# Optimization experiments

Hardware: AMD Instinct MI355X
Metric: run time of the kernel (lower is better)

Reference implementation:

```python
import jax, jax.numpy as jnp
import numpy as np

N = 50000   # nodes
E = 500000  # edges
D = 128     # enc_dim == Hout
INIT_W = 0.1


def _lin_w(k, din, dout):
    return jax.random.normal(k, (dout, din), jnp.float32) * INIT_W


def setup_inputs() -> dict:
    key = jax.random.key(0)
    ks = jax.random.split(key, 16)
    inp = {
        "x": jax.random.normal(ks[0], (N, D), jnp.float32),
        "src": jax.random.randint(ks[1], (E,), 0, N),
        "dst": jax.random.randint(ks[2], (E,), 0, N),
        # encoders (Linear enc_dim -> enc_dim)
        "WencK": _lin_w(ks[3], D, D), "bencK": jnp.zeros((D,), jnp.float32),
        "WencP1": _lin_w(ks[4], D, D), "bencP1": jnp.zeros((D,), jnp.float32),
        "WencP2": _lin_w(ks[5], D, D), "bencP2": jnp.zeros((D,), jnp.float32),
        # Kfun: Linear-Tanh-Linear-ReLU-Linear
        "K0W": _lin_w(ks[6], D, D), "K0b": jnp.zeros((D,), jnp.float32),
        "K1W": _lin_w(ks[7], D, D), "K1b": jnp.zeros((D,), jnp.float32),
        "K2W": _lin_w(ks[8], D, D), "K2b": jnp.zeros((D,), jnp.float32),
        # Ufun: Linear-Tanh-Linear-ReLU-Linear
        "U0W": _lin_w(ks[9], D, D), "U0b": jnp.zeros((D,), jnp.float32),
        "U1W": _lin_w(ks[10], D, D), "U1b": jnp.zeros((D,), jnp.float32),
        "U2W": _lin_w(ks[11], D, D), "U2b": jnp.zeros((D,), jnp.float32),
    }
    return inp


def _mlp3(h, W0, b0, W1, b1, W2, b2):
    h = jnp.tanh(h @ W0.T + b0)
    h = jax.nn.relu(h @ W1.T + b1)
    return h @ W2.T + b2


def reference(x, src, dst,
              WencK, bencK, WencP1, bencP1, WencP2, bencP2,
              K0W, K0b, K1W, K1b, K2W, K2b,
              U0W, U0b, U1W, U1b, U2W, U2b):
    # getK: encode nodes, copy_u + sum to dst, node MLP
    h1 = x @ WencK.T + bencK                                   # [N, D]
    h1_agg = jax.ops.segment_sum(h1[src], dst, num_segments=N)  # [N, D]
    Knode = _mlp3(h1_agg, K0W, K0b, K1W, K1b, K2W, K2b)         # [N, D]
    # getU: u_add_v on encoded features, edge MLP
    p1 = x @ WencP1.T + bencP1
    p2 = x @ WencP2.T + bencP2
    Eedge = _mlp3(p1[src] + p2[dst], U0W, U0b, U1W, U1b, U2W, U2b)  # [E, D]
    # getH: u_mul_e + sum to dst
    Enew = jax.ops.segment_sum(Knode[src] * Eedge, dst, num_segments=N)  # [N, D]
    return jnp.sum(Enew)
```

## Files before the change

kernel.cpp:

```cpp
#include <hip/hip_runtime.h>
#include <hip/hip_bf16.h>
#include <math.h>

#define NN 50000
#define NE 500000
#define DD 128
#define STR 136
#define NSCAN (2 * NN)
#define SCAN_BLK ((NSCAN + 1023) / 1024)
#define HIST_BLK ((NE + 255) / 256)
#define CVT_BLK  ((NN * DD + 4095) / 4096)
#define PRECONV_BLK ((7 * 2048 + 1023) / 1024)
#define ENC_BLK  ((NN + 127) / 128)

typedef __attribute__((ext_vector_type(8))) short short8;
typedef __attribute__((ext_vector_type(4))) float floatx4;

__device__ __forceinline__ float bf2f(unsigned short u) {
    unsigned v = ((unsigned)u) << 16;
    float f;
    __builtin_memcpy(&f, &v, 4);
    return f;
}
__device__ __forceinline__ unsigned short f2bf(float f) {
    unsigned x;
    __builtin_memcpy(&x, &f, 4);
    x += 0x7FFF + ((x >> 16) & 1);
    return (unsigned short)(x >> 16);
}
__device__ __forceinline__ float fast_tanh(float x) {
    float t = __builtin_amdgcn_exp2f(x * 2.88539008177793f);
    return 1.f - 2.f * __builtin_amdgcn_rcpf(t + 1.f);
}

__global__ __launch_bounds__(256) void k1_kernel(
    const int* __restrict__ src, const int* __restrict__ dst,
    int* __restrict__ cnt_dst, int* __restrict__ cnt_src,
    int* __restrict__ rank_d, int* __restrict__ rank_s,
    const float* __restrict__ x, unsigned short* __restrict__ xbf,
    const float* __restrict__ U0W, const float* __restrict__ WencP1,
    const float* __restrict__ WencP2, const float* __restrict__ K0W,
    const float* __restrict__ WencK,
    const float* __restrict__ bp1, const float* __restrict__ bp2,
    const float* __restrict__ U0b, const float* __restrict__ bk,
    const float* __restrict__ U2b,
    float* __restrict__ comp, float* __restrict__ bvecs)
{
    __shared__ float Bs[DD * DD];
    int blk = blockIdx.x;
    int t = threadIdx.x;

    if (blk < HIST_BLK) {
        int e = blk * 256 + t;
        if (e < NE) {
            rank_d[e] = atomicAdd(&cnt_dst[dst[e]], 1);
            rank_s[e] = atomicAdd(&cnt_src[src[e]], 1);
        }
        return;
    }
    if (blk < HIST_BLK + CVT_BLK) {
        int base = (blk - HIST_BLK) * 4096;
        #pragma unroll
        for (int j = 0; j < 4; ++j) {
            int idx = base + (j * 256 + t) * 4;
            if (idx < NN * DD) {
                float4 f = *(const float4*)&x[idx];
                ushort4 v4;
                v4.x = f2bf(f.x); v4.y = f2bf(f.y);
                v4.z = f2bf(f.z); v4.w = f2bf(f.w);
                *(ushort4*)&xbf[idx] = v4;
            }
        }
        return;
    }

    int b = blk - (HIST_BLK + CVT_BLK);
    if (b == 6) {
        if (t < 128) {
            float s1 = 0.f, s2 = 0.f;
            for (int k = 0; k < DD; ++k) {
                s1 += U0W[t * DD + k] * (bp1[k] + bp2[k]);
                s2 += K0W[t * DD + k] * bk[k];
            }
            bvecs[t] = s1 + U0b[t];
            bvecs[128 + t] = s2;
            int f = (t & 64) + 16 * (t & 3) + ((t & 63) >> 2);
            bvecs[256 + t] = U2b[f];
        }
        return;
    }
    int mat = b >> 1, half = b & 1;
    const float* A = (mat == 2) ? K0W : U0W;
    const float* B = (mat == 0) ? WencP1 : (mat == 1) ? WencP2 : WencK;
    float* C = comp + (size_t)mat * DD * DD;
    for (int i = 0; i < 64; ++i)
        Bs[i * 256 + t] = B[i * 256 + t];
    __syncthreads();
    int row = half * 64 + (t >> 2);
    int j0 = (t & 3) * 32;
    float acc[32];
    #pragma unroll
    for (int jj = 0; jj < 32; ++jj) acc[jj] = 0.f;
    for (int k = 0; k < DD; ++k) {
        float a = A[row * DD + k];
        #pragma unroll
        for (int jj = 0; jj < 32; ++jj)
            acc[jj] += a * Bs[k * DD + j0 + jj];
    }
    #pragma unroll
    for (int jj = 0; jj < 32; ++jj) C[row * DD + j0 + jj] = acc[jj];
}

__global__ __launch_bounds__(1024) void k2_kernel(
    const float* __restrict__ comp, const float* __restrict__ K1W,
    const float* __restrict__ K2W, const float* __restrict__ U2W,
    const float* __restrict__ U1W, unsigned short* __restrict__ wfrag,
    const int* __restrict__ cnt, int* __restrict__ base, int* __restrict__ bsum)
{
    int t = threadIdx.x;
    if (blockIdx.x < PRECONV_BLK) {
        int g = blockIdx.x * 1024 + t;
        if (g >= 7 * 2048) return;
        int m = g >> 11;
        int rem = g & 2047;
        int kt = rem >> 9, nt = (rem >> 6) & 7, lane = rem & 63;
        const float* W;
        bool perm = false, tr = false;
        switch (m) {
            case 0: W = comp; break;
            case 1: W = comp + 16384; break;
            case 2: W = comp + 32768; break;
            case 3: W = K1W; perm = true; break;
            case 4: W = K2W; perm = true; break;
            case 5: W = U2W; perm = true; tr = true; break;
            default: W = U1W; break;
        }
        int n = nt * 16 + (lane & 15);
        #pragma unroll
        for (int j = 0; j < 8; ++j) {
            int ks = kt * 32 + (lane >> 4) * 8 + j;
            int f = perm ? (ks & 64) + 16 * (ks & 3) + ((ks & 63) >> 2) : ks;
            float v = tr ? W[f * DD + n] : W[n * DD + f];
            wfrag[(size_t)g * 8 + j] = f2bf(v);
        }
        return;
    }
    __shared__ int wsum[16];
    int sb = blockIdx.x - PRECONV_BLK;
    int i = sb * 1024 + t;
    int v = (i < NSCAN) ? cnt[i] : 0;
    int lane = t & 63, w = t >> 6;
    int xv = v;
    #pragma unroll
    for (int off = 1; off < 64; off <<= 1) {
        int y = __shfl_up(xv, off);
        if (lane >= off) xv += y;
    }
    if (lane == 63) wsum[w] = xv;
    __syncthreads();
    if (w == 0) {
        int s = (lane < 16) ? wsum[lane] : 0;
        #pragma unroll
        for (int off = 1; off < 16; off <<= 1) {
            int y = __shfl_up(s, off);
            if (lane >= off) s += y;
        }
        if (lane < 16) wsum[lane] = s;
    }
    __syncthreads();
    int wavebase = (w == 0) ? 0 : wsum[w - 1];
    int incl = wavebase + xv;
    if (i < NSCAN) base[i] = incl - v;
    if (t == 1023) bsum[sb] = incl;
}

__global__ __launch_bounds__(128) void scan2_kernel(
    int* __restrict__ bsum, float* __restrict__ out)
{
    if (threadIdx.x == 0 && blockIdx.x == 0) *out = 0.f;
    __shared__ int wsum[2];
    int t = threadIdx.x;
    int v = (t < SCAN_BLK) ? bsum[t] : 0;
    int lane = t & 63, w = t >> 6;
    int x = v;
    #pragma unroll
    for (int off = 1; off < 64; off <<= 1) {
        int y = __shfl_up(x, off);
        if (lane >= off) x += y;
    }
    if (lane == 63) wsum[w] = x;
    __syncthreads();
    int wavebase = (w == 0) ? 0 : wsum[0];
    int incl = wavebase + x;
    if (t < SCAN_BLK) bsum[t] = incl - v;
}

__global__ __launch_bounds__(1024) void scan3_kernel(
    int* __restrict__ base, const int* __restrict__ bsum)
{
    int i = blockIdx.x * 1024 + threadIdx.x;
    if (i < NSCAN) base[i] += bsum[blockIdx.x];
}

__global__ __launch_bounds__(256) void place_kernel(
    const int* __restrict__ src, const int* __restrict__ dst,
    const int* __restrict__ base,
    const int* __restrict__ rank_d, const int* __restrict__ rank_s,
    int* __restrict__ sorted_src_bydst, int2* __restrict__ epairs)
{
    int e = blockIdx.x * 256 + threadIdx.x;
    if (e < NE) {
        int s = src[e], d = dst[e];
        sorted_src_bydst[base[d] + rank_d[e]] = s;
        int p = base[NN + s] + rank_s[e] - NE;
        epairs[p] = make_int2(s, d);
    }
}

__global__ __launch_bounds__(256) void agg_kernel(
    const unsigned short* __restrict__ xbf,
    const int* __restrict__ base, const int* __restrict__ cnt,
    const int* __restrict__ sorted_src,
    unsigned short* __restrict__ xagg)
{
    int wave = blockIdx.x * 4 + (threadIdx.x >> 6);
    int lane = threadIdx.x & 63;
    if (wave >= NN) return;
    int lo = base[wave];
    int hi = lo + cnt[wave];
    float ax = 0.f, ay = 0.f;
    for (int off = lo; off < hi; off += 64) {
        int myid = (off + lane < hi) ? sorted_src[off + lane] : 0;
        int nk = min(64, hi - off);
        int k = 0;
        for (; k + 4 <= nk; k += 4) {
            int s0 = __shfl(myid, k);
            int s1 = __shfl(myid, k + 1);
            int s2 = __shfl(myid, k + 2);
            int s3 = __shfl(myid, k + 3);
            ushort2 v0 = *(const ushort2*)&xbf[(size_t)s0 * DD + lane * 2];
            ushort2 v1 = *(const ushort2*)&xbf[(size_t)s1 * DD + lane * 2];
            ushort2 v2 = *(const ushort2*)&xbf[(size_t)s2 * DD + lane * 2];
            ushort2 v3 = *(const ushort2*)&xbf[(size_t)s3 * DD + lane * 2];
            ax += bf2f(v0.x) + bf2f(v1.x) + bf2f(v2.x) + bf2f(v3.x);
            ay += bf2f(v0.y) + bf2f(v1.y) + bf2f(v2.y) + bf2f(v3.y);
        }
        for (; k < nk; ++k) {
            int s = __shfl(myid, k);
            ushort2 v = *(const ushort2*)&xbf[(size_t)s * DD + lane * 2];
            ax += bf2f(v.x);
            ay += bf2f(v.y);
        }
    }
    ushort2 o;
    o.x = f2bf(ax); o.y = f2bf(ay);
    *(ushort2*)&xagg[(size_t)wave * DD + lane * 2] = o;
}

__global__ __launch_bounds__(256) void encnode_kernel(
    const float* __restrict__ x, const unsigned short* __restrict__ xagg,
    const unsigned short* __restrict__ wf, const float* __restrict__ bvecs,
    const int* __restrict__ cnt,
    const float* __restrict__ K0b, const float* __restrict__ K1b,
    const float* __restrict__ K2b,
    unsigned short* __restrict__ q1, unsigned short* __restrict__ q2,
    unsigned short* __restrict__ Km, float* __restrict__ kb)
{
    __shared__ unsigned short A[128 * STR];
    const int t = threadIdx.x;
    const int lane = t & 63, w = t >> 6;
    const int wm = w >> 1, wn = w & 1;
    const int c = lane & 15, q = lane >> 4;

    if (blockIdx.x < ENC_BLK) {
        const int row0 = blockIdx.x * 128;
        #pragma unroll
        for (int i = 0; i < 16; ++i) {
            int idx = i * 256 + t;
            int r = idx >> 5, ch = idx & 31;
            int gr = row0 + r;
            ushort4 v4 = {0, 0, 0, 0};
            if (gr < NN) {
                float4 f = *(const float4*)&x[(size_t)gr * DD + ch * 4];
                v4.x = f2bf(f.x); v4.y = f2bf(f.y);
                v4.z = f2bf(f.z); v4.w = f2bf(f.w);
            }
            *(ushort4*)&A[r * STR + ch * 4] = v4;
        }
        __syncthreads();

        for (int l = 0; l < 2; ++l) {
            floatx4 acc[4][4];
            #pragma unroll
            for (int i = 0; i < 4; ++i)
                #pragma unroll
                for (int j = 0; j < 4; ++j)
                    acc[i][j] = (floatx4){0.f, 0.f, 0.f, 0.f};
            const short8* W8 = (const short8*)(wf + (size_t)l * 16384);
            #pragma unroll
            for (int kt = 0; kt < 4; ++kt) {
                short8 af[4], bfr[4];
                #pragma unroll
                for (int i = 0; i < 4; ++i)
                    af[i] = *(const short8*)&A[(wm * 64 + i * 16 + c) * STR + kt * 32 + q * 8];
                #pragma unroll
                for (int j = 0; j < 4; ++j)
                    bfr[j] = W8[(kt * 8 + wn * 4 + j) * 64 + lane];
                #pragma unroll
                for (int i = 0; i < 4; ++i)
                    #pragma unroll
                    for (int j = 0; j < 4; ++j)
                        acc[i][j] = __builtin_amdgcn_mfma_f32_16x16x32_bf16(af[i], bfr[j], acc[i][j], 0, 0, 0);
            }
            unsigned short* pp = (l == 0) ? q1 : q2;
            float bv[4];
            #pragma unroll
            for (int j = 0; j < 4; ++j)
                bv[j] = (l == 0) ? bvecs[c + 16 * j + 64 * wn] : 0.f;

            #pragma unroll
            for (int i = 0; i < 4; ++i)
                #pragma unroll
                for (int r = 0; r < 4; ++r) {
                    int node = row0 + wm * 64 + i * 16 + 4 * q + r;
                    if (node < NN) {
                        #pragma unroll
                        for (int j = 0; j < 4; ++j)
                            pp[(size_t)node * DD + c + 16 * j + 64 * wn] = f2bf(acc[i][j][r] + bv[j]);
                    }
                }
        }
        return;
    }

    const int row0 = (blockIdx.x - ENC_BLK) * 128;
    #pragma unroll
    for (int i = 0; i < 8; ++i) {
        int idx = i * 256 + t;
        int r = idx >> 4, ch = idx & 15;
        int gr = row0 + r;
        short8 v = (short8){0,0,0,0,0,0,0,0};
        if (gr < NN) v = *(const short8*)&xagg[(size_t)gr * DD + ch * 8];
        *(short8*)&A[r * STR + ch * 8] = v;
    }
    __syncthreads();

    for (int l = 0; l < 4; ++l) {
        floatx4 acc[4][4];
        #pragma unroll
        for (int i = 0; i < 4; ++i)
            #pragma unroll
            for (int j = 0; j < 4; ++j)
                acc[i][j] = (floatx4){0.f, 0.f, 0.f, 0.f};
        const short8* W8 = (const short8*)(wf + (size_t)(2 + l) * 16384);
        #pragma unroll
        for (int kt = 0; kt < 4; ++kt) {
            short8 af[4], bfr[4];
            #pragma unroll
            for (int i = 0; i < 4; ++i)
                af[i] = *(const short8*)&A[(wm * 64 + i * 16 + c) * STR + kt * 32 + q * 8];
            #pragma unroll
            for (int j = 0; j < 4; ++j)
                bfr[j] = W8[(kt * 8 + wn * 4 + j) * 64 + lane];
            #pragma unroll
            for (int i = 0; i < 4; ++i)
                #pragma unroll
                for (int j = 0; j < 4; ++j)
                    acc[i][j] = __builtin_amdgcn_mfma_f32_16x16x32_bf16(af[i], bfr[j], acc[i][j], 0, 0, 0);
        }

        if (l < 3) {
            const float* bb = (l == 0) ? K0b : (l == 1) ? K1b : K2b;
            float bv[4];
            #pragma unroll
            for (int j = 0; j < 4; ++j) bv[j] = bb[c + 16 * j + 64 * wn];
            float bvv[4];
            #pragma unroll
            for (int j = 0; j < 4; ++j)
                bvv[j] = (l == 0) ? bvecs[128 + c + 16 * j + 64 * wn] : 0.f;

            __syncthreads();
            #pragma unroll
            for (int i = 0; i < 4; ++i)
                #pragma unroll
                for (int r = 0; r < 4; ++r) {
                    int node = row0 + wm * 64 + i * 16 + 4 * q + r;
                    float cn = (l == 0) ? (float)((node < NN) ? cnt[node] : 0) : 0.f;
                    float v0 = acc[i][0][r] + bv[0] + cn * bvv[0];
                    float v1 = acc[i][1][r] + bv[1] + cn * bvv[1];
                    float v2 = acc[i][2][r] + bv[2] + cn * bvv[2];
                    float v3 = acc[i][3][r] + bv[3] + cn * bvv[3];
                    if (l == 0) {
                        v0 = fast_tanh(v0); v1 = fast_tanh(v1);
                        v2 = fast_tanh(v2); v3 = fast_tanh(v3);
                    } else if (l == 1) {
                        v0 = fmaxf(v0, 0.f); v1 = fmaxf(v1, 0.f);
                        v2 = fmaxf(v2, 0.f); v3 = fmaxf(v3, 0.f);
                    }
                    ushort4 pk;
                    pk.x = f2bf(v0); pk.y = f2bf(v1); pk.z = f2bf(v2); pk.w = f2bf(v3);
                    int m = wm * 64 + i * 16 + 4 * q + r;
                    *(ushort4*)&A[m * STR + 4 * c + 64 * wn] = pk;
                }
            __syncthreads();

            if (l == 2) {
                if (t < 128) {
                    int node = row0 + t;
                    if (node < NN) {
                        float s = 0.f;
                        #pragma unroll
                        for (int ch = 0; ch < 16; ++ch) {
                            short8 v = *(const short8*)&A[t * STR + ch * 8];
                            #pragma unroll
                            for (int e = 0; e < 8; ++e)
                                s += bf2f((unsigned short)v[e]) * bvecs[256 + ch * 8 + e];
                        }
                        kb[node] = s;
                    }
                }
            }
        } else {
            #pragma unroll
            for (int i = 0; i < 4; ++i)
                #pragma unroll
                for (int r = 0; r < 4; ++r) {
                    int node = row0 + wm * 64 + i * 16 + 4 * q + r;
                    if (node < NN) {
                        ushort4 pk;
                        pk.x = f2bf(acc[i][0][r]);
                        pk.y = f2bf(acc[i][1][r]);
                        pk.z = f2bf(acc[i][2][r]);
                        pk.w = f2bf(acc[i][3][r]);
                        *(ushort4*)&Km[(size_t)node * DD + 4 * c + 64 * wn] = pk;
                    }
                }
        }
    }
}

__global__ __launch_bounds__(256) void edge_kernel(
    const unsigned short* __restrict__ q1, const unsigned short* __restrict__ q2,
    const unsigned short* __restrict__ Km, const float* __restrict__ kb,
    const int2* __restrict__ epairs,
    const unsigned short* __restrict__ wf, const float* __restrict__ U1b,
    float* __restrict__ out)
{
    __shared__ unsigned short A[128 * STR];
    __shared__ int sidx[128];
    __shared__ int didx[128];
    __shared__ float red[4];
    const int t = threadIdx.x;
    const int lane = t & 63, w = t >> 6;
    const int wm = w >> 1, wn = w & 1;
    const int c = lane & 15, q = lane >> 4;

    float bv[4];
    #pragma unroll
    for (int j = 0; j < 4; ++j) bv[j] = U1b[c + 16 * j + 64 * wn];

    float part = 0.f;

    for (int tile = 0; tile < 2; ++tile) {
        const int e0 = blockIdx.x * 256 + tile * 128;
        if (tile) __syncthreads();
        if (t < 128) {
            int e = e0 + t;
            if (e < NE) {
                int2 p = epairs[e];
                sidx[t] = p.x;
                didx[t] = p.y;
            } else {
                sidx[t] = -1;
                didx[t] = 0;
            }
        }
        __syncthreads();

        if (t < 128 && sidx[t] >= 0) part += kb[sidx[t]];

        #pragma unroll
        for (int i = 0; i < 8; ++i) {
            int idx = i * 256 + t;
            int r = idx >> 4, ch = idx & 15;
            int s = sidx[r];
            int o32[4] = {0, 0, 0, 0};
            if (s >= 0) {
                short8 a8 = *(const short8*)&q1[(size_t)s * DD + ch * 8];
                short8 b8 = *(const short8*)&q2[(size_t)didx[r] * DD + ch * 8];
                #pragma unroll
                for (int k = 0; k < 8; k += 2) {
                    float2 u;
                    u.x = fast_tanh(bf2f((unsigned short)a8[k])     + bf2f((unsigned short)b8[k]));
                    u.y = fast_tanh(bf2f((unsigned short)a8[k + 1]) + bf2f((unsigned short)b8[k + 1]));
                    __hip_bfloat162 hb = __float22bfloat162_rn(u);
                    __builtin_memcpy(&o32[k >> 1], &hb, 4);
                }
            }
            *(int4*)&A[r * STR + ch * 8] = *(int4*)o32;
        }
        __syncthreads();

        floatx4 acc[4][4];
        #pragma unroll
        for (int i = 0; i < 4; ++i)
            #pragma unroll
            for (int j = 0; j < 4; ++j)
                acc[i][j] = (floatx4){0.f, 0.f, 0.f, 0.f};
        const short8* W8 = (const short8*)(wf + (size_t)6 * 16384);
        #pragma unroll
        for (int kt = 0; kt < 4; ++kt) {
            short8 af[4], bfr[4];
            #pragma unroll
            for (int i = 0; i < 4; ++i)
                af[i] = *(const short8*)&A[(wm * 64 + i * 16 + c) * STR + kt * 32 + q * 8];
            #pragma unroll
            for (int j = 0; j < 4; ++j)
                bfr[j] = W8[(kt * 8 + wn * 4 + j) * 64 + lane];
            #pragma unroll
            for (int i = 0; i < 4; ++i)
                #pragma unroll
                for (int j = 0; j < 4; ++j)
                    acc[i][j] = __builtin_amdgcn_mfma_f32_16x16x32_bf16(af[i], bfr[j], acc[i][j], 0, 0, 0);
        }

        #pragma unroll
        for (int i = 0; i < 4; ++i)
            #pragma unroll
            for (int r = 0; r < 4; ++r) {
                int m = wm * 64 + i * 16 + 4 * q + r;
                int s = sidx[m];
                if (s >= 0) {
                    ushort4 km4 = *(const ushort4*)&Km[(size_t)s * DD + 4 * c + 64 * wn];
                    part += fmaxf(acc[i][0][r] + bv[0], 0.f) * bf2f(km4.x)
                          + fmaxf(acc[i][1][r] + bv[1], 0.f) * bf2f(km4.y)
                          + fmaxf(acc[i][2][r] + bv[2], 0.f) * bf2f(km4.z)
                          + fmaxf(acc[i][3][r] + bv[3], 0.f) * bf2f(km4.w);
                }
            }
    }

    #pragma unroll
    for (int off = 32; off > 0; off >>= 1)
        part += __shfl_down(part, off);
    if (lane == 0) red[w] = part;
    __syncthreads();
    if (t == 0)
        atomicAdd(out, red[0] + red[1] + red[2] + red[3]);
}

extern "C" void kernel_launch(void* const* d_in, const int* in_sizes, int n_in,
                              void* d_out, int out_size, void* d_ws, size_t ws_size,
                              hipStream_t stream)
{
    const float* x     = (const float*)d_in[0];
    const int*   src   = (const int*)  d_in[1];
    const int*   dst   = (const int*)  d_in[2];
    const float* WencK = (const float*)d_in[3];
    const float* bencK = (const float*)d_in[4];
    const float* WencP1= (const float*)d_in[5];
    const float* bencP1= (const float*)d_in[6];
    const float* WencP2= (const float*)d_in[7];
    const float* bencP2= (const float*)d_in[8];
    const float* K0W   = (const float*)d_in[9];
    const float* K0b   = (const float*)d_in[10];
    const float* K1W   = (const float*)d_in[11];
    const float* K1b   = (const float*)d_in[12];
    const float* K2W   = (const float*)d_in[13];
    const float* K2b   = (const float*)d_in[14];
    const float* U0W   = (const float*)d_in[15];
    const float* U0b   = (const float*)d_in[16];
    const float* U1W   = (const float*)d_in[17];
    const float* U1b   = (const float*)d_in[18];
    const float* U2W   = (const float*)d_in[19];
    const float* U2b   = (const float*)d_in[20];

    char* ws = (char*)d_ws;
    unsigned short* wfrag = (unsigned short*)ws;
    float* comp  = (float*)(ws + 0x40000);
    float* bvecs = (float*)(ws + 0x70000);
    unsigned short* xbf  = (unsigned short*)(ws + 0x71000);
    unsigned short* q1   = xbf + (size_t)NN * DD;
    unsigned short* q2   = q1 + (size_t)NN * DD;
    unsigned short* Kmg  = q2 + (size_t)NN * DD;
    unsigned short* xagg = Kmg + (size_t)NN * DD;
    float* kb       = (float*)(xagg + (size_t)NN * DD);
    int* cnt_dst    = (int*)(kb + NN);
    int* cnt_src    = cnt_dst + NN;
    int* base       = cnt_src + NN;
    int* bsum       = base + NSCAN;
    int* rank_d     = bsum + 128;
    int* rank_s     = rank_d + NE;
    int* sorted_src_bydst = rank_s + NE;
    int2* epairs    = (int2*)(sorted_src_bydst + NE);

    hipMemsetAsync(cnt_dst, 0, 2 * NN * sizeof(int), stream);

    k1_kernel<<<HIST_BLK + CVT_BLK + 7, 256, 0, stream>>>(
        src, dst, cnt_dst, cnt_src, rank_d, rank_s, x, xbf,
        U0W, WencP1, WencP2, K0W, WencK, bencP1, bencP2, U0b, bencK, U2b,
        comp, bvecs);

    k2_kernel<<<PRECONV_BLK + SCAN_BLK, 1024, 0, stream>>>(
        comp, K1W, K2W, U2W, U1W, wfrag, cnt_dst, base, bsum);

    scan2_kernel<<<1, 128, 0, stream>>>(bsum, (float*)d_out);
    scan3_kernel<<<SCAN_BLK, 1024, 0, stream>>>(base, bsum);

    place_kernel<<<HIST_BLK, 256, 0, stream>>>(
        src, dst, base, rank_d, rank_s, sorted_src_bydst, epairs);

    agg_kernel<<<(NN + 3) / 4, 256, 0, stream>>>(
        xbf, base, cnt_dst, sorted_src_bydst, xagg);

    encnode_kernel<<<2 * ENC_BLK, 256, 0, stream>>>(
        x, xagg, wfrag, bvecs, cnt_dst, K0b, K1b, K2b, q1, q2, Kmg, kb);

    edge_kernel<<<(NE + 255) / 256, 256, 0, stream>>>(
        q1, q2, Kmg, kb, epairs, wfrag, U1b, (float*)d_out);
}
```

Before: 340.7 us.

## Fold scan fixup into consumers, co-schedule aggregation with encoder, retile node/edge kernels

Drops the separate scan3 kernel, so place and aggregation read base plus the per-block prefix directly. The aggregation gather is merged into the same launch as the P1/P2 encoder GEMM blocks so the two independent workloads run concurrently. The node MLP moves to its own 64-row, 128-thread kernel for more blocks. The edge kernel now handles one 128-edge tile per block instead of two. The trade-off is fewer launches and better overlap against extra bsum loads and more edge blocks with repeated weight-fragment loads.

```diff
diff --git a/kernel.cpp b/kernel.cpp
--- a/kernel.cpp
+++ b/kernel.cpp
@@ -12,6 +12,8 @@
 #define CVT_BLK  ((NN * DD + 4095) / 4096)
 #define PRECONV_BLK ((7 * 2048 + 1023) / 1024)
 #define ENC_BLK  ((NN + 127) / 128)
+#define AGG_BLK  ((NN + 3) / 4)
+#define NODE_BLK ((NN + 63) / 64)
 
 typedef __attribute__((ext_vector_type(8))) short short8;
 typedef __attribute__((ext_vector_type(4))) float floatx4;
@@ -195,148 +197,146 @@
     if (t < SCAN_BLK) bsum[t] = incl - v;
 }
 
-__global__ __launch_bounds__(1024) void scan3_kernel(
-    int* __restrict__ base, const int* __restrict__ bsum)
-{
-    int i = blockIdx.x * 1024 + threadIdx.x;
-    if (i < NSCAN) base[i] += bsum[blockIdx.x];
-}
-
 __global__ __launch_bounds__(256) void place_kernel(
     const int* __restrict__ src, const int* __restrict__ dst,
-    const int* __restrict__ base,
+    const int* __restrict__ base, const int* __restrict__ bsum,
     const int* __restrict__ rank_d, const int* __restrict__ rank_s,
     int* __restrict__ sorted_src_bydst, int2* __restrict__ epairs)
 {
     int e = blockIdx.x * 256 + threadIdx.x;
     if (e < NE) {
         int s = src[e], d = dst[e];
-        sorted_src_bydst[base[d] + rank_d[e]] = s;
-        int p = base[NN + s] + rank_s[e] - NE;
+        sorted_src_bydst[base[d] + bsum[d >> 10] + rank_d[e]] = s;
+        int si = NN + s;
+        int p = base[si] + bsum[si >> 10] + rank_s[e] - NE;
         epairs[p] = make_int2(s, d);
     }
 }
 
-__global__ __launch_bounds__(256) void agg_kernel(
-    const unsigned short* __restrict__ xbf,
-    const int* __restrict__ base, const int* __restrict__ cnt,
-    const int* __restrict__ sorted_src,
+__global__ __launch_bounds__(256) void aggenc_kernel(
+    const float* __restrict__ x, const unsigned short* __restrict__ xbf,
+    const unsigned short* __restrict__ wf, const float* __restrict__ bvecs,
+    const int* __restrict__ base, const int* __restrict__ bsum,
+    const int* __restrict__ cnt, const int* __restrict__ sorted_src,
+    unsigned short* __restrict__ q1, unsigned short* __restrict__ q2,
     unsigned short* __restrict__ xagg)
-{
-    int wave = blockIdx.x * 4 + (threadIdx.x >> 6);
-    int lane = threadIdx.x & 63;
-    if (wave >= NN) return;
-    int lo = base[wave];
-    int hi = lo + cnt[wave];
-    float ax = 0.f, ay = 0.f;
-    for (int off = lo; off < hi; off += 64) {
-        int myid = (off + lane < hi) ? sorted_src[off + lane] : 0;
-        int nk = min(64, hi - off);
-        int k = 0;
-        for (; k + 4 <= nk; k += 4) {
-            int s0 = __shfl(myid, k);
-            int s1 = __shfl(myid, k + 1);
-            int s2 = __shfl(myid, k + 2);
-            int s3 = __shfl(myid, k + 3);
-            ushort2 v0 = *(const ushort2*)&xbf[(size_t)s0 * DD + lane * 2];
-            ushort2 v1 = *(const ushort2*)&xbf[(size_t)s1 * DD + lane * 2];
-            ushort2 v2 = *(const ushort2*)&xbf[(size_t)s2 * DD + lane * 2];
-            ushort2 v3 = *(const ushort2*)&xbf[(size_t)s3 * DD + lane * 2];
-            ax += bf2f(v0.x) + bf2f(v1.x) + bf2f(v2.x) + bf2f(v3.x);
-            ay += bf2f(v0.y) + bf2f(v1.y) + bf2f(v2.y) + bf2f(v3.y);
-        }
-        for (; k < nk; ++k) {
-            int s = __shfl(myid, k);
-            ushort2 v = *(const ushort2*)&xbf[(size_t)s * DD + lane * 2];
-            ax += bf2f(v.x);
-            ay += bf2f(v.y);
-        }
-    }
-    ushort2 o;
-    o.x = f2bf(ax); o.y = f2bf(ay);
-    *(ushort2*)&xagg[(size_t)wave * DD + lane * 2] = o;
-}
-
-__global__ __launch_bounds__(256) void encnode_kernel(
-    const float* __restrict__ x, const unsigned short* __restrict__ xagg,
-    const unsigned short* __restrict__ wf, const float* __restrict__ bvecs,
-    const int* __restrict__ cnt,
-    const float* __restrict__ K0b, const float* __restrict__ K1b,
-    const float* __restrict__ K2b,
-    unsigned short* __restrict__ q1, unsigned short* __restrict__ q2,
-    unsigned short* __restrict__ Km, float* __restrict__ kb)
 {
     __shared__ unsigned short A[128 * STR];
     const int t = threadIdx.x;
     const int lane = t & 63, w = t >> 6;
+
+    if (blockIdx.x >= ENC_BLK) {
+        int node = (blockIdx.x - ENC_BLK) * 4 + w;
+        if (node >= NN) return;
+        int lo = base[node] + bsum[node >> 10];
+        int hi = lo + cnt[node];
+        float ax = 0.f, ay = 0.f;
+        for (int off = lo; off < hi; off += 64) {
+            int myid = (off + lane < hi) ? sorted_src[off + lane] : 0;
+            int nk = min(64, hi - off);
+            int k = 0;
+            for (; k + 4 <= nk; k += 4) {
+                int s0 = __shfl(myid, k);
+                int s1 = __shfl(myid, k + 1);
+                int s2 = __shfl(myid, k + 2);
+                int s3 = __shfl(myid, k + 3);
+                ushort2 v0 = *(const ushort2*)&xbf[(size_t)s0 * DD + lane * 2];
+                ushort2 v1 = *(const ushort2*)&xbf[(size_t)s1 * DD + lane * 2];
+                ushort2 v2 = *(const ushort2*)&xbf[(size_t)s2 * DD + lane * 2];
+                ushort2 v3 = *(const ushort2*)&xbf[(size_t)s3 * DD + lane * 2];
+                ax += bf2f(v0.x) + bf2f(v1.x) + bf2f(v2.x) + bf2f(v3.x);
+                ay += bf2f(v0.y) + bf2f(v1.y) + bf2f(v2.y) + bf2f(v3.y);
+            }
+            for (; k < nk; ++k) {
+                int s = __shfl(myid, k);
+                ushort2 v = *(const ushort2*)&xbf[(size_t)s * DD + lane * 2];
+                ax += bf2f(v.x);
+                ay += bf2f(v.y);
+            }
+        }
+        ushort2 o;
+        o.x = f2bf(ax); o.y = f2bf(ay);
+        *(ushort2*)&xagg[(size_t)node * DD + lane * 2] = o;
+        return;
+    }
+
     const int wm = w >> 1, wn = w & 1;
     const int c = lane & 15, q = lane >> 4;
-
-    if (blockIdx.x < ENC_BLK) {
-        const int row0 = blockIdx.x * 128;
-        #pragma unroll
-        for (int i = 0; i < 16; ++i) {
-            int idx = i * 256 + t;
-            int r = idx >> 5, ch = idx & 31;
-            int gr = row0 + r;
-            ushort4 v4 = {0, 0, 0, 0};
-            if (gr < NN) {
-                float4 f = *(const float4*)&x[(size_t)gr * DD + ch * 4];
-                v4.x = f2bf(f.x); v4.y = f2bf(f.y);
-                v4.z = f2bf(f.z); v4.w = f2bf(f.w);
-            }
-            *(ushort4*)&A[r * STR + ch * 4] = v4;
-        }
-        __syncthreads();
-
-        for (int l = 0; l < 2; ++l) {
-            floatx4 acc[4][4];
+    const int row0 = blockIdx.x * 128;
+    #pragma unroll
+    for (int i = 0; i < 16; ++i) {
+        int idx = i * 256 + t;
+        int r = idx >> 5, ch = idx & 31;
+        int gr = row0 + r;
+        ushort4 v4 = {0, 0, 0, 0};
+        if (gr < NN) {
+            float4 f = *(const float4*)&x[(size_t)gr * DD + ch * 4];
+            v4.x = f2bf(f.x); v4.y = f2bf(f.y);
+            v4.z = f2bf(f.z); v4.w = f2bf(f.w);
+        }
+        *(ushort4*)&A[r * STR + ch * 4] = v4;
+    }
+    __syncthreads();
+
+    for (int l = 0; l < 2; ++l) {
+        floatx4 acc[4][4];
+        #pragma unroll
+        for (int i = 0; i < 4; ++i)
+            #pragma unroll
+            for (int j = 0; j < 4; ++j)
+                acc[i][j] = (floatx4){0.f, 0.f, 0.f, 0.f};
+        const short8* W8 = (const short8*)(wf + (size_t)l * 16384);
+        #pragma unroll
+        for (int kt = 0; kt < 4; ++kt) {
+            short8 af[4], bfr[4];
+            #pragma unroll
+            for (int i = 0; i < 4; ++i)
+                af[i] = *(const short8*)&A[(wm * 64 + i * 16 + c) * STR + kt * 32 + q * 8];
+            #pragma unroll
+            for (int j = 0; j < 4; ++j)
+                bfr[j] = W8[(kt * 8 + wn * 4 + j) * 64 + lane];
             #pragma unroll
             for (int i = 0; i < 4; ++i)
                 #pragma unroll
                 for (int j = 0; j < 4; ++j)
-                    acc[i][j] = (floatx4){0.f, 0.f, 0.f, 0.f};
-            const short8* W8 = (const short8*)(wf + (size_t)l * 16384);
-            #pragma unroll
-            for (int kt = 0; kt < 4; ++kt) {
-                short8 af[4], bfr[4];
-                #pragma unroll
-                for (int i = 0; i < 4; ++i)
-                    af[i] = *(const short8*)&A[(wm * 64 + i * 16 + c) * STR + kt * 32 + q * 8];
-                #pragma unroll
-                for (int j = 0; j < 4; ++j)
-                    bfr[j] = W8[(kt * 8 + wn * 4 + j) * 64 + lane];
-                #pragma unroll
-                for (int i = 0; i < 4; ++i)
+                    acc[i][j] = __builtin_amdgcn_mfma_f32_16x16x32_bf16(af[i], bfr[j], acc[i][j], 0, 0, 0);
+        }
+        unsigned short* pp = (l == 0) ? q1 : q2;
+        float bv[4];
+        #pragma unroll
+        for (int j = 0; j < 4; ++j)
+            bv[j] = (l == 0) ? bvecs[c + 16 * j + 64 * wn] : 0.f;
+
+        #pragma unroll
+        for (int i = 0; i < 4; ++i)
+            #pragma unroll
+            for (int r = 0; r < 4; ++r) {
+                int node = row0 + wm * 64 + i * 16 + 4 * q + r;
+                if (node < NN) {
                     #pragma unroll
                     for (int j = 0; j < 4; ++j)
-                        acc[i][j] = __builtin_amdgcn_mfma_f32_16x16x32_bf16(af[i], bfr[j], acc[i][j], 0, 0, 0);
-            }
-            unsigned short* pp = (l == 0) ? q1 : q2;
-            float bv[4];
-            #pragma unroll
-            for (int j = 0; j < 4; ++j)
-                bv[j] = (l == 0) ? bvecs[c + 16 * j + 64 * wn] : 0.f;
-
-            #pragma unroll
-            for (int i = 0; i < 4; ++i)
-                #pragma unroll
-                for (int r = 0; r < 4; ++r) {
-                    int node = row0 + wm * 64 + i * 16 + 4 * q + r;
-                    if (node < NN) {
-                        #pragma unroll
-                        for (int j = 0; j < 4; ++j)
-                            pp[(size_t)node * DD + c + 16 * j + 64 * wn] = f2bf(acc[i][j][r] + bv[j]);
-                    }
+                        pp[(size_t)node * DD + c + 16 * j + 64 * wn] = f2bf(acc[i][j][r] + bv[j]);
                 }
-        }
-        return;
-    }
-
-    const int row0 = (blockIdx.x - ENC_BLK) * 128;
+            }
+    }
+}
+
+__global__ __launch_bounds__(128) void node_kernel(
+    const unsigned short* __restrict__ xagg, const unsigned short* __restrict__ wf,
+    const int* __restrict__ cnt, const float* __restrict__ bvecs,
+    const float* __restrict__ K0b, const float* __restrict__ K1b,
+    const float* __restrict__ K2b,
+    unsigned short* __restrict__ Km, float* __restrict__ kb)
+{
+    __shared__ unsigned short A[64 * STR];
+    const int t = threadIdx.x;
+    const int lane = t & 63, wn = t >> 6;
+    const int c = lane & 15, q = lane >> 4;
+    const int row0 = blockIdx.x * 64;
+
     #pragma unroll
     for (int i = 0; i < 8; ++i) {
-        int idx = i * 256 + t;
+        int idx = i * 128 + t;
         int r = idx >> 4, ch = idx & 15;
         int gr = row0 + r;
         short8 v = (short8){0,0,0,0,0,0,0,0};
@@ -358,7 +358,7 @@
             short8 af[4], bfr[4];
             #pragma unroll
             for (int i = 0; i < 4; ++i)
-                af[i] = *(const short8*)&A[(wm * 64 + i * 16 + c) * STR + kt * 32 + q * 8];
+                af[i] = *(const short8*)&A[(i * 16 + c) * STR + kt * 32 + q * 8];
             #pragma unroll
             for (int j = 0; j < 4; ++j)
                 bfr[j] = W8[(kt * 8 + wn * 4 + j) * 64 + lane];
@@ -384,7 +384,7 @@
             for (int i = 0; i < 4; ++i)
                 #pragma unroll
                 for (int r = 0; r < 4; ++r) {
-                    int node = row0 + wm * 64 + i * 16 + 4 * q + r;
+                    int node = row0 + i * 16 + 4 * q + r;
                     float cn = (l == 0) ? (float)((node < NN) ? cnt[node] : 0) : 0.f;
                     float v0 = acc[i][0][r] + bv[0] + cn * bvv[0];
                     float v1 = acc[i][1][r] + bv[1] + cn * bvv[1];
@@ -399,13 +399,13 @@
                     }
                     ushort4 pk;
                     pk.x = f2bf(v0); pk.y = f2bf(v1); pk.z = f2bf(v2); pk.w = f2bf(v3);
-                    int m = wm * 64 + i * 16 + 4 * q + r;
+                    int m = i * 16 + 4 * q + r;
                     *(ushort4*)&A[m * STR + 4 * c + 64 * wn] = pk;
                 }
             __syncthreads();
 
             if (l == 2) {
-                if (t < 128) {
+                if (t < 64) {
                     int node = row0 + t;
                     if (node < NN) {
                         float s = 0.f;
@@ -425,7 +425,7 @@
             for (int i = 0; i < 4; ++i)
                 #pragma unroll
                 for (int r = 0; r < 4; ++r) {
-                    int node = row0 + wm * 64 + i * 16 + 4 * q + r;
+                    int node = row0 + i * 16 + 4 * q + r;
                     if (node < NN) {
                         ushort4 pk;
                         pk.x = f2bf(acc[i][0][r]);
@@ -454,91 +454,86 @@
     const int lane = t & 63, w = t >> 6;
     const int wm = w >> 1, wn = w & 1;
     const int c = lane & 15, q = lane >> 4;
-
+    const int e0 = blockIdx.x * 128;
+
+    if (t < 128) {
+        int e = e0 + t;
+        if (e < NE) {
+            int2 p = epairs[e];
+            sidx[t] = p.x;
+            didx[t] = p.y;
+        } else {
+            sidx[t] = -1;
+            didx[t] = 0;
+        }
+    }
+    __syncthreads();
+
+    float part = 0.f;
+    if (t < 128 && sidx[t] >= 0) part += kb[sidx[t]];
+
+    #pragma unroll
+    for (int i = 0; i < 8; ++i) {
+        int idx = i * 256 + t;
+        int r = idx >> 4, ch = idx & 15;
+        int s = sidx[r];
+        int o32[4] = {0, 0, 0, 0};
+        if (s >= 0) {
+            short8 a8 = *(const short8*)&q1[(size_t)s * DD + ch * 8];
+            short8 b8 = *(const short8*)&q2[(size_t)didx[r] * DD + ch * 8];
+            #pragma unroll
+            for (int k = 0; k < 8; k += 2) {
+                float2 u;
+                u.x = fast_tanh(bf2f((unsigned short)a8[k])     + bf2f((unsigned short)b8[k]));
+                u.y = fast_tanh(bf2f((unsigned short)a8[k + 1]) + bf2f((unsigned short)b8[k + 1]));
+                __hip_bfloat162 hb = __float22bfloat162_rn(u);
+                __builtin_memcpy(&o32[k >> 1], &hb, 4);
+            }
+        }
+        *(int4*)&A[r * STR + ch * 8] = *(int4*)o32;
+    }
+    __syncthreads();
+
+    floatx4 acc[4][4];
+    #pragma unroll
+    for (int i = 0; i < 4; ++i)
+        #pragma unroll
+        for (int j = 0; j < 4; ++j)
+            acc[i][j] = (floatx4){0.f, 0.f, 0.f, 0.f};
+    const short8* W8 = (const short8*)(wf + (size_t)6 * 16384);
+    #pragma unroll
+    for (int kt = 0; kt < 4; ++kt) {
+        short8 af[4], bfr[4];
+        #pragma unroll
+        for (int i = 0; i < 4; ++i)
+            af[i] = *(const short8*)&A[(wm * 64 + i * 16 + c) * STR + kt * 32 + q * 8];
+        #pragma unroll
+        for (int j = 0; j < 4; ++j)
+            bfr[j] = W8[(kt * 8 + wn * 4 + j) * 64 + lane];
+        #pragma unroll
+        for (int i = 0; i < 4; ++i)
+            #pragma unroll
+            for (int j = 0; j < 4; ++j)
+                acc[i][j] = __builtin_amdgcn_mfma_f32_16x16x32_bf16(af[i], bfr[j], acc[i][j], 0, 0, 0);
+    }
     float bv[4];
     #pragma unroll
     for (int j = 0; j < 4; ++j) bv[j] = U1b[c + 16 * j + 64 * wn];
 
-    float part = 0.f;
-
-    for (int tile = 0; tile < 2; ++tile) {
-        const int e0 = blockIdx.x * 256 + tile * 128;
-        if (tile) __syncthreads();
-        if (t < 128) {
-            int e = e0 + t;
-            if (e < NE) {
-                int2 p = epairs[e];
-                sidx[t] = p.x;
-                didx[t] = p.y;
-            } else {
-                sidx[t] = -1;
-                didx[t] = 0;
-            }
-        }
-        __syncthreads();
-
-        if (t < 128 && sidx[t] >= 0) part += kb[sidx[t]];
-
-        #pragma unroll
-        for (int i = 0; i < 8; ++i) {
-            int idx = i * 256 + t;
-            int r = idx >> 4, ch = idx & 15;
-            int s = sidx[r];
-            int o32[4] = {0, 0, 0, 0};
+    #pragma unroll
+    for (int i = 0; i < 4; ++i)
+        #pragma unroll
+        for (int r = 0; r < 4; ++r) {
+            int m = wm * 64 + i * 16 + 4 * q + r;
+            int s = sidx[m];
             if (s >= 0) {
-                short8 a8 = *(const short8*)&q1[(size_t)s * DD + ch * 8];
-                short8 b8 = *(const short8*)&q2[(size_t)didx[r] * DD + ch * 8];
-                #pragma unroll
-                for (int k = 0; k < 8; k += 2) {
-                    float2 u;
-                    u.x = fast_tanh(bf2f((unsigned short)a8[k])     + bf2f((unsigned short)b8[k]));
-                    u.y = fast_tanh(bf2f((unsigned short)a8[k + 1]) + bf2f((unsigned short)b8[k + 1]));
-                    __hip_bfloat162 hb = __float22bfloat162_rn(u);
-                    __builtin_memcpy(&o32[k >> 1], &hb, 4);
-                }
-            }
-            *(int4*)&A[r * STR + ch * 8] = *(int4*)o32;
-        }
-        __syncthreads();
-
-        floatx4 acc[4][4];
-        #pragma unroll
-        for (int i = 0; i < 4; ++i)
-            #pragma unroll
-            for (int j = 0; j < 4; ++j)
-                acc[i][j] = (floatx4){0.f, 0.f, 0.f, 0.f};
-        const short8* W8 = (const short8*)(wf + (size_t)6 * 16384);
-        #pragma unroll
-        for (int kt = 0; kt < 4; ++kt) {
-            short8 af[4], bfr[4];
-            #pragma unroll
-            for (int i = 0; i < 4; ++i)
-                af[i] = *(const short8*)&A[(wm * 64 + i * 16 + c) * STR + kt * 32 + q * 8];
-            #pragma unroll
-            for (int j = 0; j < 4; ++j)
-                bfr[j] = W8[(kt * 8 + wn * 4 + j) * 64 + lane];
-            #pragma unroll
-            for (int i = 0; i < 4; ++i)
-                #pragma unroll
-                for (int j = 0; j < 4; ++j)
-                    acc[i][j] = __builtin_amdgcn_mfma_f32_16x16x32_bf16(af[i], bfr[j], acc[i][j], 0, 0, 0);
-        }
-
-        #pragma unroll
-        for (int i = 0; i < 4; ++i)
-            #pragma unroll
-            for (int r = 0; r < 4; ++r) {
-                int m = wm * 64 + i * 16 + 4 * q + r;
-                int s = sidx[m];
-                if (s >= 0) {
-                    ushort4 km4 = *(const ushort4*)&Km[(size_t)s * DD + 4 * c + 64 * wn];
-                    part += fmaxf(acc[i][0][r] + bv[0], 0.f) * bf2f(km4.x)
-                          + fmaxf(acc[i][1][r] + bv[1], 0.f) * bf2f(km4.y)
-                          + fmaxf(acc[i][2][r] + bv[2], 0.f) * bf2f(km4.z)
-                          + fmaxf(acc[i][3][r] + bv[3], 0.f) * bf2f(km4.w);
-                }
-            }
-    }
+                ushort4 km4 = *(const ushort4*)&Km[(size_t)s * DD + 4 * c + 64 * wn];
+                part += fmaxf(acc[i][0][r] + bv[0], 0.f) * bf2f(km4.x)
+                      + fmaxf(acc[i][1][r] + bv[1], 0.f) * bf2f(km4.y)
+                      + fmaxf(acc[i][2][r] + bv[2], 0.f) * bf2f(km4.z)
+                      + fmaxf(acc[i][3][r] + bv[3], 0.f) * bf2f(km4.w);
+            }
+        }
 
     #pragma unroll
     for (int off = 32; off > 0; off >>= 1)
@@ -605,17 +600,17 @@
         comp, K1W, K2W, U2W, U1W, wfrag, cnt_dst, base, bsum);
 
     scan2_kernel<<<1, 128, 0, stream>>>(bsum, (float*)d_out);
-    scan3_kernel<<<SCAN_BLK, 1024, 0, stream>>>(base, bsum);
 
     place_kernel<<<HIST_BLK, 256, 0, stream>>>(
-        src, dst, base, rank_d, rank_s, sorted_src_bydst, epairs);
-
-    agg_kernel<<<(NN + 3) / 4, 256, 0, stream>>>(
-        xbf, base, cnt_dst, sorted_src_bydst, xagg);
-
-    encnode_kernel<<<2 * ENC_BLK, 256, 0, stream>>>(
-        x, xagg, wfrag, bvecs, cnt_dst, K0b, K1b, K2b, q1, q2, Kmg, kb);
-
-    edge_kernel<<<(NE + 255) / 256, 256, 0, stream>>>(
+        src, dst, base, bsum, rank_d, rank_s, sorted_src_bydst, epairs);
+
+    aggenc_kernel<<<ENC_BLK + AGG_BLK, 256, 0, stream>>>(
+        x, xbf, wfrag, bvecs, base, bsum, cnt_dst, sorted_src_bydst,
+        q1, q2, xagg);
+
+    node_kernel<<<NODE_BLK, 128, 0, stream>>>(
+        xagg, wfrag, cnt_dst, bvecs, K0b, K1b, K2b, Kmg, kb);
+
+    edge_kernel<<<(NE + 127) / 128, 256, 0, stream>>>(
         q1, q2, Kmg, kb, epairs, wfrag, U1b, (float*)d_out);
 }
```

Result: slower. 377.5 us (+10.8%).
